# Performance work log

Hardware: AMD Instinct MI355X
Metric: run time of the kernel (lower is better)

The kernel has to match this reference:

```python
import jax, jax.numpy as jnp
import numpy as np

NU, NI, DIN, DOUT, NS, E = 100000, 100000, 128, 128, 5, 500000


def setup_inputs() -> dict:
    key = jax.random.key(0)
    ks = jax.random.split(key, 9)
    scale = 1.0 / np.sqrt(DIN)
    return {
        "user_inputs": jax.random.normal(ks[0], (NU, DIN), jnp.float32),
        "item_inputs": jax.random.normal(ks[1], (NI, DIN), jnp.float32),
        "weight": jax.random.normal(ks[2], (DIN, DOUT, NS), jnp.float32) * scale,
        "u_rows": jax.random.randint(ks[3], (NS, E), 0, NU),
        "u_cols": jax.random.randint(ks[4], (NS, E), 0, NI),
        "u_vals": jax.random.uniform(ks[5], (NS, E), jnp.float32),
        "i_rows": jax.random.randint(ks[6], (NS, E), 0, NI),
        "i_cols": jax.random.randint(ks[7], (NS, E), 0, NU),
        "i_vals": jax.random.uniform(ks[8], (NS, E), jnp.float32),
    }


def _spmm(rows, cols, vals, dense, n_rows):
    # COO sparse [n_rows, n_cols] @ dense [n_cols, d] -> [n_rows, d]
    msgs = vals[:, None] * dense[cols]  # [E, d]
    return jax.ops.segment_sum(msgs, rows, num_segments=n_rows)


def reference(user_inputs, item_inputs, weight, u_rows, u_cols, u_vals, i_rows, i_cols, i_vals):
    n_users = user_inputs.shape[0]
    n_items = item_inputs.shape[0]
    num_support = weight.shape[-1]
    w = jnp.zeros(weight.shape[:2], weight.dtype)
    user_hidden = jnp.zeros((n_users, weight.shape[1]), weight.dtype)
    item_hidden = jnp.zeros((n_items, weight.shape[1]), weight.dtype)
    for i in range(num_support):  # fixed small structural loop (5 rating levels)
        w = w + weight[..., i]            # cumulative weight sum, as in original
        tmp_u = user_inputs @ w           # [NU, DOUT]
        tmp_v = item_inputs @ w           # [NI, DOUT]
        user_hidden = user_hidden + _spmm(u_rows[i], u_cols[i], u_vals[i], tmp_v, n_users)
        item_hidden = item_hidden + _spmm(i_rows[i], i_cols[i], i_vals[i], tmp_u, n_items)
    return jax.nn.relu(user_hidden), jax.nn.relu(item_hidden)
```

## Files before the change

### kernel.cpp

```cpp
#include <hip/hip_runtime.h>

#define R_     100000
#define NSUP   5
#define EDGES  500000
#define D_     128
#define ND     (NSUP * D_)
#define BR     64
#define PPS2   ((R_ + BR - 1) / BR)
#define NPART2 (NSUP * PPS2)
#define NBINS2 (2 * NPART2)
#define CAP2   512

#define PB     977

using short8 = __attribute__((ext_vector_type(8))) short;
using f32x4  = __attribute__((ext_vector_type(4))) float;

static __device__ __forceinline__ float bf2f_lo(unsigned p) { return __uint_as_float(p << 16); }
static __device__ __forceinline__ float bf2f_hi(unsigned p) { return __uint_as_float(p & 0xffff0000u); }
static __device__ __forceinline__ unsigned short f2bf(float x) {
    unsigned u = __float_as_uint(x);
    return (unsigned short)((u + 0x7fffu + ((u >> 16) & 1u)) >> 16);
}

__global__ __launch_bounds__(256) void prep_k(const float* __restrict__ user_in,
                                              const float* __restrict__ item_in,
                                              const float* __restrict__ w,
                                              unsigned short* __restrict__ srcb,
                                              unsigned short* __restrict__ bt,
                                              int* __restrict__ curs) {
    int b = blockIdx.x, tid = threadIdx.x;
    if (b < 25000) {
        int side = b / 12500;
        int t = (b - side * 12500) * 256 + tid;
        const float* src = side ? user_in : item_in;
        float4 v = *(const float4*)(src + (size_t)t * 4);
        ushort4 o;
        o.x = f2bf(v.x); o.y = f2bf(v.y); o.z = f2bf(v.z); o.w = f2bf(v.w);
        *(ushort4*)(srcb + (size_t)side * (R_ * D_) + (size_t)t * 4) = o;
    } else if (b < 25320) {
        int t = (b - 25000) * 256 + tid;
        int o = t / ND;
        int kk = t - o * ND;
        int i = kk >> 7, d = kk & 127;
        float s = 0.f;
        for (int j = 0; j <= i; j++) s += w[(d * D_ + o) * NSUP + j];
        bt[t] = f2bf(s);
    } else {
        int t = (b - 25320) * 256 + tid;
        if (t < NBINS2) curs[t] = 0;
    }
}

__global__ __launch_bounds__(512) void place_k(const int* __restrict__ u_rows,
                                               const int* __restrict__ u_cols,
                                               const float* __restrict__ u_vals,
                                               const int* __restrict__ i_rows,
                                               const int* __restrict__ i_cols,
                                               const float* __restrict__ i_vals,
                                               int* __restrict__ curs,
                                               uint2* __restrict__ cedge) {
    int seg = blockIdx.x % 10;
    int wb  = blockIdx.x / 10;
    int e = wb * 512 + threadIdx.x;
    if (e >= EDGES) return;
    int side = seg / NSUP;
    int sup  = seg - side * NSUP;
    const int*   rows = side ? i_rows : u_rows;
    const int*   cols = side ? i_cols : u_cols;
    const float* vals = side ? i_vals : u_vals;
    int idx = sup * EDGES + e;
    int row = rows[idx];
    int bin = side * NPART2 + sup * PPS2 + (row >> 6);
    int pos = atomicAdd(&curs[bin], 1);
    if (pos < CAP2) {
        uint2 E;
        E.x = (unsigned)cols[idx] | ((unsigned)(row & 63) << 17);
        E.y = __float_as_uint(vals[idx]);
        cedge[(size_t)bin * CAP2 + pos] = E;
    }
}

__global__ __launch_bounds__(256) void fused_k(const int* __restrict__ curs,
                                               const uint2* __restrict__ cedge,
                                               const unsigned short* __restrict__ srcb,
                                               const unsigned short* __restrict__ BT,
                                               float* __restrict__ out) {
    __shared__ uint2 eraw[CAP2];
    __shared__ uint2 eds[CAP2];
    __shared__ int rcnt[BR];
    __shared__ int rsc[BR];
    __shared__ unsigned short stile[BR * D_];

    int side = blockIdx.x / PPS2;
    int bin  = blockIdx.x - side * PPS2;
    const unsigned short* srcbf = srcb + (size_t)side * (R_ * D_);
    float* outp = out + (size_t)side * R_ * D_;

    int tid = threadIdx.x;
    int wid = tid >> 6, lane = tid & 63;
    int g = lane >> 4, l16 = lane & 15;

    f32x4 acc[4][2];
#pragma unroll
    for (int rt = 0; rt < 4; rt++)
#pragma unroll
        for (int nt = 0; nt < 2; nt++)
            acc[rt][nt] = (f32x4){0.f, 0.f, 0.f, 0.f};

    for (int i = 0; i < NSUP; i++) {
        int p = side * NPART2 + i * PPS2 + bin;
        size_t st = (size_t)p * CAP2;
        int n = curs[p];
        if (n > CAP2) n = CAP2;

        if (tid < BR) rcnt[tid] = 0;
        __syncthreads();
        for (int e = tid; e < n; e += 256) {
            uint2 E = cedge[st + e];
            eraw[e] = E;
            atomicAdd(&rcnt[(E.x >> 17) & 63], 1);
        }
        __syncthreads();
        if (wid == 0) {
            int vv = rcnt[lane];
            int s = vv;
#pragma unroll
            for (int off = 1; off < 64; off <<= 1) {
                int u = __shfl_up(s, off, 64);
                if (lane >= off) s += u;
            }
            rsc[lane] = s;
            rcnt[lane] = s - vv;
        }
        __syncthreads();
        for (int e = tid; e < n; e += 256) {
            uint2 E = eraw[e];
            int pos = atomicAdd(&rcnt[(E.x >> 17) & 63], 1);
            eds[pos] = E;
        }
        __syncthreads();

        for (int rq = wid; rq < 16; rq += 4) {
            int r = rq * 4 + g;
            int s0 = r ? rsc[r - 1] : 0;
            int e2 = rsc[r];
            float a0 = 0.f, a1 = 0.f, a2 = 0.f, a3 = 0.f;
            float a4 = 0.f, a5 = 0.f, a6 = 0.f, a7 = 0.f;
            int e = s0;
            for (; e + 3 < e2; e += 4) {
                uint2 E0 = eds[e], E1 = eds[e + 1], E2 = eds[e + 2], E3 = eds[e + 3];
                const uint4 p0 = *(const uint4*)(srcbf + (size_t)(E0.x & 0x1FFFFu) * D_ + l16 * 8);
                const uint4 p1 = *(const uint4*)(srcbf + (size_t)(E1.x & 0x1FFFFu) * D_ + l16 * 8);
                const uint4 p2 = *(const uint4*)(srcbf + (size_t)(E2.x & 0x1FFFFu) * D_ + l16 * 8);
                const uint4 p3 = *(const uint4*)(srcbf + (size_t)(E3.x & 0x1FFFFu) * D_ + l16 * 8);
                float v0 = __uint_as_float(E0.y), v1 = __uint_as_float(E1.y);
                float v2 = __uint_as_float(E2.y), v3 = __uint_as_float(E3.y);
                a0 += v0 * bf2f_lo(p0.x); a1 += v0 * bf2f_hi(p0.x);
                a2 += v0 * bf2f_lo(p0.y); a3 += v0 * bf2f_hi(p0.y);
                a4 += v0 * bf2f_lo(p0.z); a5 += v0 * bf2f_hi(p0.z);
                a6 += v0 * bf2f_lo(p0.w); a7 += v0 * bf2f_hi(p0.w);
                a0 += v1 * bf2f_lo(p1.x); a1 += v1 * bf2f_hi(p1.x);
                a2 += v1 * bf2f_lo(p1.y); a3 += v1 * bf2f_hi(p1.y);
                a4 += v1 * bf2f_lo(p1.z); a5 += v1 * bf2f_hi(p1.z);
                a6 += v1 * bf2f_lo(p1.w); a7 += v1 * bf2f_hi(p1.w);
                a0 += v2 * bf2f_lo(p2.x); a1 += v2 * bf2f_hi(p2.x);
                a2 += v2 * bf2f_lo(p2.y); a3 += v2 * bf2f_hi(p2.y);
                a4 += v2 * bf2f_lo(p2.z); a5 += v2 * bf2f_hi(p2.z);
                a6 += v2 * bf2f_lo(p2.w); a7 += v2 * bf2f_hi(p2.w);
                a0 += v3 * bf2f_lo(p3.x); a1 += v3 * bf2f_hi(p3.x);
                a2 += v3 * bf2f_lo(p3.y); a3 += v3 * bf2f_hi(p3.y);
                a4 += v3 * bf2f_lo(p3.z); a5 += v3 * bf2f_hi(p3.z);
                a6 += v3 * bf2f_lo(p3.w); a7 += v3 * bf2f_hi(p3.w);
            }
            for (; e < e2; e++) {
                uint2 E = eds[e];
                const uint4 pk = *(const uint4*)(srcbf + (size_t)(E.x & 0x1FFFFu) * D_ + l16 * 8);
                float vv = __uint_as_float(E.y);
                a0 += vv * bf2f_lo(pk.x); a1 += vv * bf2f_hi(pk.x);
                a2 += vv * bf2f_lo(pk.y); a3 += vv * bf2f_hi(pk.y);
                a4 += vv * bf2f_lo(pk.z); a5 += vv * bf2f_hi(pk.z);
                a6 += vv * bf2f_lo(pk.w); a7 += vv * bf2f_hi(pk.w);
            }
            uint4 P;
            P.x = ((unsigned)f2bf(a1) << 16) | f2bf(a0);
            P.y = ((unsigned)f2bf(a3) << 16) | f2bf(a2);
            P.z = ((unsigned)f2bf(a5) << 16) | f2bf(a4);
            P.w = ((unsigned)f2bf(a7) << 16) | f2bf(a6);
            int boff = r * 256 + ((l16 * 16) ^ ((r & 7) << 4));
            *(uint4*)((char*)stile + boff) = P;
        }
        __syncthreads();

        const unsigned short* btp = BT + (size_t)i * D_;
#pragma unroll
        for (int cc = 0; cc < 4; cc++) {
            short8 afr[4];
#pragma unroll
            for (int rt = 0; rt < 4; rt++) {
                int row = rt * 16 + l16;
                int boff = row * 256 + ((cc * 64 + g * 16) ^ ((row & 7) << 4));
                afr[rt] = *(const short8*)((const char*)stile + boff);
            }
#pragma unroll
            for (int nt = 0; nt < 2; nt++) {
                short8 b = *(const short8*)(btp + (size_t)(wid * 32 + nt * 16 + l16) * ND
                                            + cc * 32 + g * 8);
#pragma unroll
                for (int rt = 0; rt < 4; rt++)
                    acc[rt][nt] = __builtin_amdgcn_mfma_f32_16x16x32_bf16(afr[rt], b,
                                                                          acc[rt][nt], 0, 0, 0);
            }
        }
    }

#pragma unroll
    for (int nt = 0; nt < 2; nt++) {
#pragma unroll
        for (int rt = 0; rt < 4; rt++) {
#pragma unroll
            for (int rr = 0; rr < 4; rr++) {
                int grow = bin * BR + rt * 16 + g * 4 + rr;
                if (grow < R_) {
                    int col = wid * 32 + nt * 16 + l16;
                    float v = acc[rt][nt][rr];
                    outp[(size_t)grow * D_ + col] = v > 0.f ? v : 0.f;
                }
            }
        }
    }
}

extern "C" void kernel_launch(void* const* d_in, const int* in_sizes, int n_in,
                              void* d_out, int out_size, void* d_ws, size_t ws_size,
                              hipStream_t stream) {
    const float* user_in = (const float*)d_in[0];
    const float* item_in = (const float*)d_in[1];
    const float* weight  = (const float*)d_in[2];
    const int* u_rows = (const int*)d_in[3];
    const int* u_cols = (const int*)d_in[4];
    const float* u_vals = (const float*)d_in[5];
    const int* i_rows = (const int*)d_in[6];
    const int* i_cols = (const int*)d_in[7];
    const float* i_vals = (const float*)d_in[8];
    float* out = (float*)d_out;

    char* ws = (char*)d_ws;
    unsigned short* srcb = (unsigned short*)(ws);
    unsigned short* BT   = (unsigned short*)(ws + 51200000);
    uint2* cedge         = (uint2*)         (ws + 51363840);
    int*   curs          = (int*)           (ws + 115384320);

    prep_k<<<25382, 256, 0, stream>>>(user_in, item_in, weight, srcb, BT, curs);
    place_k<<<10 * PB, 512, 0, stream>>>(u_rows, u_cols, u_vals,
                                         i_rows, i_cols, i_vals, curs, cedge);
    fused_k<<<2 * PPS2, 256, 0, stream>>>(curs, cedge, srcb, BT, out);
}
```

Baseline: 610.3 us.

## Replace global atomic edge binning with block-local counting sort and offset table

Edge bucketing now uses per-block counting sort: each block histograms 8192 edges in LDS, scans, writes sorted edges contiguously plus a per-bin offset table. The fused kernel gathers its 64-row bin's edges from all 62 source chunks using those offsets instead of reading one fixed-capacity global bin. This removes global atomics and scattered writes, and the counter zeroing step, in exchange for a larger offset table and a more fragmented gather in the consumer. LDS for the raw edge staging is aliased onto the source tile buffer.

```diff
diff --git a/kernel.cpp b/kernel.cpp
--- a/kernel.cpp
+++ b/kernel.cpp
@@ -7,11 +7,12 @@
 #define ND     (NSUP * D_)
 #define BR     64
 #define PPS2   ((R_ + BR - 1) / BR)
-#define NPART2 (NSUP * PPS2)
-#define NBINS2 (2 * NPART2)
+#define NBIN1  PPS2
 #define CAP2   512
 
-#define PB     977
+#define EPB    8192
+#define BPS    62
+#define OROWS  1568
 
 using short8 = __attribute__((ext_vector_type(8))) short;
 using f32x4  = __attribute__((ext_vector_type(4))) float;
@@ -27,8 +28,7 @@
                                               const float* __restrict__ item_in,
                                               const float* __restrict__ w,
                                               unsigned short* __restrict__ srcb,
-                                              unsigned short* __restrict__ bt,
-                                              int* __restrict__ curs) {
+                                              unsigned short* __restrict__ bt) {
     int b = blockIdx.x, tid = threadIdx.x;
     if (b < 25000) {
         int side = b / 12500;
@@ -38,7 +38,7 @@
         ushort4 o;
         o.x = f2bf(v.x); o.y = f2bf(v.y); o.z = f2bf(v.z); o.w = f2bf(v.w);
         *(ushort4*)(srcb + (size_t)side * (R_ * D_) + (size_t)t * 4) = o;
-    } else if (b < 25320) {
+    } else {
         int t = (b - 25000) * 256 + tid;
         int o = t / ND;
         int kk = t - o * ND;
@@ -46,51 +46,94 @@
         float s = 0.f;
         for (int j = 0; j <= i; j++) s += w[(d * D_ + o) * NSUP + j];
         bt[t] = f2bf(s);
-    } else {
-        int t = (b - 25320) * 256 + tid;
-        if (t < NBINS2) curs[t] = 0;
-    }
-}
-
-__global__ __launch_bounds__(512) void place_k(const int* __restrict__ u_rows,
-                                               const int* __restrict__ u_cols,
-                                               const float* __restrict__ u_vals,
-                                               const int* __restrict__ i_rows,
-                                               const int* __restrict__ i_cols,
-                                               const float* __restrict__ i_vals,
-                                               int* __restrict__ curs,
-                                               uint2* __restrict__ cedge) {
-    int seg = blockIdx.x % 10;
-    int wb  = blockIdx.x / 10;
-    int e = wb * 512 + threadIdx.x;
-    if (e >= EDGES) return;
+    }
+}
+
+__global__ __launch_bounds__(512) void place2_k(const int* __restrict__ u_rows,
+                                                const int* __restrict__ u_cols,
+                                                const float* __restrict__ u_vals,
+                                                const int* __restrict__ i_rows,
+                                                const int* __restrict__ i_cols,
+                                                const float* __restrict__ i_vals,
+                                                int* __restrict__ offs2,
+                                                uint2* __restrict__ cedge2) {
+    __shared__ int   hist[NBIN1];
+    __shared__ int   part[512];
+    __shared__ uint2 estage[EPB];
+
+    int seg = blockIdx.x / BPS;
+    int bb  = blockIdx.x - seg * BPS;
     int side = seg / NSUP;
     int sup  = seg - side * NSUP;
     const int*   rows = side ? i_rows : u_rows;
     const int*   cols = side ? i_cols : u_cols;
     const float* vals = side ? i_vals : u_vals;
-    int idx = sup * EDGES + e;
-    int row = rows[idx];
-    int bin = side * NPART2 + sup * PPS2 + (row >> 6);
-    int pos = atomicAdd(&curs[bin], 1);
-    if (pos < CAP2) {
+    int e0 = bb * EPB;
+    int ecnt = EDGES - e0; if (ecnt > EPB) ecnt = EPB;
+    size_t gb = (size_t)sup * EDGES + e0;
+    int tid = threadIdx.x;
+
+    for (int b = tid; b < NBIN1; b += 512) hist[b] = 0;
+    __syncthreads();
+    for (int e = tid; e < ecnt; e += 512)
+        atomicAdd(&hist[rows[gb + e] >> 6], 1);
+    __syncthreads();
+    int b0 = tid * 4, s4 = 0;
+    if (b0 < NBIN1) {
+#pragma unroll
+        for (int k = 0; k < 4; k++)
+            if (b0 + k < NBIN1) s4 += hist[b0 + k];
+    }
+    part[tid] = s4;
+    __syncthreads();
+    for (int off = 1; off < 512; off <<= 1) {
+        int u = (tid >= off) ? part[tid - off] : 0;
+        __syncthreads();
+        part[tid] += u;
+        __syncthreads();
+    }
+    int ex = part[tid] - s4;
+    int orow = seg * OROWS;
+    if (b0 < NBIN1) {
+        int run = ex;
+#pragma unroll
+        for (int k = 0; k < 4; k++) {
+            int b = b0 + k;
+            if (b < NBIN1) {
+                int c = hist[b];
+                offs2[(size_t)(orow + b) * 64 + bb] = run;
+                hist[b] = run;
+                run += c;
+            }
+        }
+    }
+    if (tid == 0) offs2[(size_t)(orow + NBIN1) * 64 + bb] = ecnt;
+    __syncthreads();
+    for (int e = tid; e < ecnt; e += 512) {
+        int r = rows[gb + e];
+        int pos = atomicAdd(&hist[r >> 6], 1);
         uint2 E;
-        E.x = (unsigned)cols[idx] | ((unsigned)(row & 63) << 17);
-        E.y = __float_as_uint(vals[idx]);
-        cedge[(size_t)bin * CAP2 + pos] = E;
-    }
-}
-
-__global__ __launch_bounds__(256) void fused_k(const int* __restrict__ curs,
-                                               const uint2* __restrict__ cedge,
+        E.x = (unsigned)cols[gb + e] | ((unsigned)(r & 63) << 17);
+        E.y = __float_as_uint(vals[gb + e]);
+        estage[pos] = E;
+    }
+    __syncthreads();
+    size_t cbase = (size_t)(seg * BPS + bb) * EPB;
+    for (int e = tid; e < ecnt; e += 512) cedge2[cbase + e] = estage[e];
+}
+
+__global__ __launch_bounds__(256) void fused_k(const int* __restrict__ offs2,
+                                               const uint2* __restrict__ cedge2,
                                                const unsigned short* __restrict__ srcb,
                                                const unsigned short* __restrict__ BT,
                                                float* __restrict__ out) {
-    __shared__ uint2 eraw[CAP2];
+    __shared__ unsigned short stile[BR * D_];
     __shared__ uint2 eds[CAP2];
     __shared__ int rcnt[BR];
     __shared__ int rsc[BR];
-    __shared__ unsigned short stile[BR * D_];
+    __shared__ int rstart[BPS + 1];
+    __shared__ int ro0[BPS];
+    uint2* eraw = (uint2*)&stile[0];
 
     int side = blockIdx.x / PPS2;
     int bin  = blockIdx.x - side * PPS2;
@@ -109,18 +152,41 @@
             acc[rt][nt] = (f32x4){0.f, 0.f, 0.f, 0.f};
 
     for (int i = 0; i < NSUP; i++) {
-        int p = side * NPART2 + i * PPS2 + bin;
-        size_t st = (size_t)p * CAP2;
-        int n = curs[p];
-        if (n > CAP2) n = CAP2;
-
-        if (tid < BR) rcnt[tid] = 0;
-        __syncthreads();
-        for (int e = tid; e < n; e += 256) {
-            uint2 E = cedge[st + e];
-            eraw[e] = E;
-            atomicAdd(&rcnt[(E.x >> 17) & 63], 1);
-        }
+        int seg = side * NSUP + i;
+        __syncthreads();
+        if (wid == 0) {
+            int o0v = 0, cnt = 0;
+            if (lane < BPS) {
+                const int* orow = offs2 + ((size_t)seg * OROWS + bin) * 64;
+                o0v = orow[lane];
+                cnt = orow[lane + 64] - o0v;
+            }
+            int s = cnt;
+#pragma unroll
+            for (int off = 1; off < 64; off <<= 1) {
+                int u = __shfl_up(s, off, 64);
+                if (lane >= off) s += u;
+            }
+            if (lane < BPS) { rstart[lane] = s - cnt; ro0[lane] = o0v; }
+            if (lane == BPS - 1) rstart[BPS] = s;
+        } else if (wid == 1 && lane < BR) {
+            rcnt[lane] = 0;
+        }
+        __syncthreads();
+        int n = rstart[BPS]; if (n > CAP2) n = CAP2;
+        if (tid < 4 * BPS) {
+            int rb = tid >> 2, j0 = tid & 3;
+            int rs = rstart[rb];
+            int cnt = rstart[rb + 1] - rs;
+            const uint2* src = cedge2 + (size_t)(seg * BPS + rb) * EPB + ro0[rb];
+            for (int j = j0; j < cnt; j += 4) {
+                int pos = rs + j;
+                if (pos < CAP2) eraw[pos] = src[j];
+            }
+        }
+        __syncthreads();
+        for (int e = tid; e < n; e += 256)
+            atomicAdd(&rcnt[(eraw[e].x >> 17) & 63], 1);
         __syncthreads();
         if (wid == 0) {
             int vv = rcnt[lane];
@@ -248,11 +314,11 @@
     char* ws = (char*)d_ws;
     unsigned short* srcb = (unsigned short*)(ws);
     unsigned short* BT   = (unsigned short*)(ws + 51200000);
-    uint2* cedge         = (uint2*)         (ws + 51363840);
-    int*   curs          = (int*)           (ws + 115384320);
-
-    prep_k<<<25382, 256, 0, stream>>>(user_in, item_in, weight, srcb, BT, curs);
-    place_k<<<10 * PB, 512, 0, stream>>>(u_rows, u_cols, u_vals,
-                                         i_rows, i_cols, i_vals, curs, cedge);
-    fused_k<<<2 * PPS2, 256, 0, stream>>>(curs, cedge, srcb, BT, out);
-}
+    uint2* cedge2        = (uint2*)         (ws + 51363840);
+    int*   offs2         = (int*)           (ws + 91996160);
+
+    prep_k<<<25320, 256, 0, stream>>>(user_in, item_in, weight, srcb, BT);
+    place2_k<<<10 * BPS, 512, 0, stream>>>(u_rows, u_cols, u_vals,
+                                           i_rows, i_cols, i_vals, offs2, cedge2);
+    fused_k<<<2 * PPS2, 256, 0, stream>>>(offs2, cedge2, srcb, BT, out);
+}
```

New measurement: 590.7 us. 3.2% less time.
